# Kernel tuning notes

Hardware: AMD Instinct MI355X
Metric: run time of the kernel (lower is better)

The kernel has to match this reference:

```python
import jax, jax.numpy as jnp
import numpy as np
from math import sqrt

EPS = 1e-5
N_BISECT = 30

def _entmax15_impl(x):
    # alpha=1.5 entmax along last axis via bisection (entmax_bisect, alpha=1.5)
    xs = x * 0.5  # (alpha-1) * x
    mx = jnp.max(xs, axis=-1, keepdims=True)
    d = xs.shape[-1]
    lo = mx - 1.0
    hi = mx - d ** -0.5  # d^{-(alpha-1)}
    def body(i, carry):
        lo, hi = carry
        mid = 0.5 * (lo + hi)
        f = jnp.sum(jnp.square(jnp.maximum(xs - mid, 0.0)), -1, keepdims=True) - 1.0
        lo = jnp.where(f > 0, mid, lo)
        hi = jnp.where(f > 0, hi, mid)
        return lo, hi
    lo, hi = jax.lax.fori_loop(0, N_BISECT, body, (lo, hi))
    tau = 0.5 * (lo + hi)
    p = jnp.square(jnp.maximum(xs - tau, 0.0))
    return p / jnp.sum(p, -1, keepdims=True)

@jax.custom_vjp
def entmax15(x):
    return _entmax15_impl(x)

def _entmax15_fwd(x):
    p = _entmax15_impl(x)
    return p, p

def _entmax15_bwd(p, g):
    # exact entmax-1.5 backward (entmax repo): gppr = sqrt(p) on support
    s = jnp.sqrt(p)
    dx = g * s
    q = jnp.sum(dx, -1, keepdims=True) / jnp.sum(s, -1, keepdims=True)
    return (dx - q * s,)

entmax15.defvjp(_entmax15_fwd, _entmax15_bwd)

def layer_norm(x, g, b):
    m = jnp.mean(x, -1, keepdims=True)
    v = jnp.var(x, -1, keepdims=True)
    return (x - m) / jnp.sqrt(v + EPS) * g + b

def mlp(x, w1, b1, w2, b2):
    return jax.nn.gelu(x @ w1 + b1, approximate=False) @ w2 + b2

def hopfield_core(q_in, k_in, H, wq, bq, wk, bk, wv, bv, wo, bo):
    # Faithful to Hopfield.forward with mix=True; `values` arg of the torch
    # module is ignored (it recomputes value_projection(key_projection(keys))).
    B, L, _ = q_in.shape
    S = k_in.shape[1]
    q = (q_in @ wq + bq).reshape(B, L, H, -1)
    k = k_in @ wk + bk
    v = (k @ wv + bv).reshape(B, S, H, -1)
    kh = k.reshape(B, S, H, -1)
    E = q.shape[-1]
    scores = jnp.einsum('blhe,bshe->bhls', q, kh) * (1.0 / sqrt(E))
    A = entmax15(scores)
    out = jnp.einsum('bhls,bshd->blhd', A, v)
    # mix=True: transpose(2,1) then view(B, L, -1) on contiguous (B,H,L,D)
    out = jnp.transpose(out, (0, 2, 1, 3)).reshape(B, L, -1)
    return out @ wo + bo

def _forward(n_heads, x, ct_wq, ct_bq, ct_wk, ct_bk, ct_wv, ct_bv, ct_wo, ct_bo,
             cs_wq, cs_bq, cs_wk, cs_bk, cs_wv, cs_bv, cs_wo, cs_bo, cs_key,
             hp_wq, hp_bq, hp_wk, hp_bk, hp_wv, hp_bv, hp_wo, hp_bo,
             n1_g, n1_b, n2_g, n2_b, n3_g, n3_b, n4_g, n4_b,
             m1_w1, m1_b1, m1_w2, m1_b2, m2_w1, m2_b1, m2_w2, m2_b2):
    b, ts_d, seg, d = x.shape
    time_in = x.reshape(b * ts_d, seg, d)
    time_enc = hopfield_core(time_in, time_in, n_heads,
                             ct_wq, ct_bq, ct_wk, ct_bk, ct_wv, ct_bv, ct_wo, ct_bo)
    dim_in = layer_norm(time_in + time_enc, n1_g, n1_b)
    dim_in = layer_norm(dim_in + mlp(dim_in, m1_w1, m1_b1, m1_w2, m1_b2), n2_g, n2_b)
    # '(b ts_d) seg d -> (b seg) ts_d d'
    series_in = dim_in.reshape(b, ts_d, seg, d).transpose(0, 2, 1, 3).reshape(b * seg, ts_d, d)
    # HopfieldPooling: learned stored patterns as keys
    pooled_keys = jnp.broadcast_to(cs_key, (b * seg,) + cs_key.shape[1:])
    series_h = hopfield_core(series_in, pooled_keys, n_heads,
                             cs_wq, cs_bq, cs_wk, cs_bk, cs_wv, cs_bv, cs_wo, cs_bo)
    pooled_h = hopfield_core(series_in, series_in, n_heads,
                             hp_wq, hp_bq, hp_wk, hp_bk, hp_wv, hp_bv, hp_wo, hp_bo)
    dim_enc = layer_norm(series_h + pooled_h, n3_g, n3_b)
    dim_enc = layer_norm(dim_enc + mlp(dim_enc, m2_w1, m2_b1, m2_w2, m2_b2), n4_g, n4_b)
    # '(b seg) ts_d d -> b ts_d seg d'
    return dim_enc.reshape(b, seg, ts_d, d).transpose(0, 2, 1, 3)

def setup_inputs() -> dict:
    b, ts_d, seg, d, h, dff, factor = 8, 32, 64, 1024, 16, 4096, 10
    keys = iter(jax.random.split(jax.random.key(0), 64))
    def rn(shape, s=0.02):
        return jax.random.normal(next(keys), shape, jnp.float32) * s
    inp = {"x": jax.random.normal(next(keys), (b, ts_d, seg, d), jnp.float32)}
    for p in ("ct", "cs", "hp"):
        inp[p + "_wq"] = rn((d, d)); inp[p + "_bq"] = rn((d,))
        inp[p + "_wk"] = rn((d, d)); inp[p + "_bk"] = rn((d,))
        inp[p + "_wv"] = rn((d, d)); inp[p + "_bv"] = rn((d,))
        inp[p + "_wo"] = rn((d, d)); inp[p + "_bo"] = rn((d,))
    inp["cs_key"] = rn((1, factor, d), 0.1)
    for i in ("1", "2", "3", "4"):
        inp["n" + i + "_g"] = jnp.ones((d,), jnp.float32)
        inp["n" + i + "_b"] = jnp.zeros((d,), jnp.float32)
    for m in ("m1", "m2"):
        inp[m + "_w1"] = rn((d, dff)); inp[m + "_b1"] = rn((dff,))
        inp[m + "_w2"] = rn((dff, d)); inp[m + "_b2"] = rn((d,))
    inp["n_heads"] = h
    return inp

def reference(x, ct_wq, ct_bq, ct_wk, ct_bk, ct_wv, ct_bv, ct_wo, ct_bo,
              cs_wq, cs_bq, cs_wk, cs_bk, cs_wv, cs_bv, cs_wo, cs_bo, cs_key,
              hp_wq, hp_bq, hp_wk, hp_bk, hp_wv, hp_bv, hp_wo, hp_bo,
              n1_g, n1_b, n2_g, n2_b, n3_g, n3_b, n4_g, n4_b,
              m1_w1, m1_b1, m1_w2, m1_b2, m2_w1, m2_b1, m2_w2, m2_b2, n_heads):
    return _forward(n_heads, x, ct_wq, ct_bq, ct_wk, ct_bk, ct_wv, ct_bv, ct_wo, ct_bo,
                    cs_wq, cs_bq, cs_wk, cs_bk, cs_wv, cs_bv, cs_wo, cs_bo, cs_key,
                    hp_wq, hp_bq, hp_wk, hp_bk, hp_wv, hp_bv, hp_wo, hp_bo,
                    n1_g, n1_b, n2_g, n2_b, n3_g, n3_b, n4_g, n4_b,
                    m1_w1, m1_b1, m1_w2, m1_b2, m2_w1, m2_b1, m2_w2, m2_b2)
```

## Files before the change

### kernel.cpp

```cpp
#include <hip/hip_runtime.h>
#include <cstdio>

typedef __bf16 bf16x8 __attribute__((ext_vector_type(8)));
typedef float f32x4 __attribute__((ext_vector_type(4)));
typedef int i32x4 __attribute__((ext_vector_type(4)));
typedef unsigned short u16x4 __attribute__((ext_vector_type(4)));

__device__ __forceinline__ float bf2f(unsigned short u) {
  union { unsigned int i; float f; } x; x.i = ((unsigned int)u) << 16; return x.f;
}
__device__ __forceinline__ unsigned short f2bf(float f) {
  union { float f; unsigned int i; } x; x.f = f;
  unsigned int r = x.i + 0x7fffu + ((x.i >> 16) & 1u);
  return (unsigned short)(r >> 16);
}

__device__ __forceinline__ void gl2lds16(const unsigned short* g, unsigned short* l) {
  __builtin_amdgcn_global_load_lds((const __attribute__((address_space(1))) unsigned int*)g,
                                   (__attribute__((address_space(3))) unsigned int*)l, 16, 0, 0);
}

__global__ __launch_bounds__(256) void k_cast(const float* __restrict__ in,
                                              unsigned short* __restrict__ out, int n4) {
  int i = blockIdx.x * 256 + threadIdx.x;
  if (i >= n4) return;
  f32x4 v = ((const f32x4*)in)[i];
  u16x4 o;
  o[0] = f2bf(v[0]); o[1] = f2bf(v[1]); o[2] = f2bf(v[2]); o[3] = f2bf(v[3]);
  ((u16x4*)out)[i] = o;
}

__global__ __launch_bounds__(256) void k_tcast(const float* __restrict__ src,
                                               unsigned short* __restrict__ dst,
                                               int K, int N) {
  __shared__ float tile[32][33];
  int gx = blockIdx.x * 32;
  int gy = blockIdx.y * 32;
  int t = threadIdx.x;
  int c = t & 31, r0 = t >> 5;
#pragma unroll
  for (int i = 0; i < 4; i++) {
    int r = r0 + i * 8;
    tile[r][c] = src[(size_t)(gy + r) * N + gx + c];
  }
  __syncthreads();
#pragma unroll
  for (int i = 0; i < 4; i++) {
    int r = r0 + i * 8;
    dst[(size_t)(gx + r) * K + gy + c] = f2bf(tile[c][r]);
  }
}

template <bool GELU>
__global__ __launch_bounds__(256) void k_gemm(const unsigned short* __restrict__ A,
                                              const unsigned short* __restrict__ Bt,
                                              const float* __restrict__ bias,
                                              unsigned short* __restrict__ C,
                                              int M, int N, int K) {
  __shared__ unsigned short As[2][128 * 32];
  __shared__ unsigned short Bs[2][128 * 32];
  const int rowA0 = blockIdx.y * 128, colB0 = blockIdx.x * 128;
  const int t = threadIdx.x, w = t >> 6, lane = t & 63;
  const int wr = w >> 1, wc = w & 1;
  const int srow = w * 16 + (lane >> 2);
  const unsigned short* pa = A + (size_t)(rowA0 + srow) * K + (lane & 3) * 8;
  const unsigned short* pb = Bt + (size_t)(colB0 + srow) * K + (lane & 3) * 8;
  const size_t row64 = (size_t)64 * K;

  f32x4 acc[4][4] = {};
  const int ka = (lane >> 4) * 8, ra = lane & 15;

  auto stage = [&](int buf, int kk) {
    gl2lds16(pa + kk,         &As[buf][w * 512]);
    gl2lds16(pa + row64 + kk, &As[buf][2048 + w * 512]);
    gl2lds16(pb + kk,         &Bs[buf][w * 512]);
    gl2lds16(pb + row64 + kk, &Bs[buf][2048 + w * 512]);
  };
  stage(0, 0);
  int buf = 0;
  for (int kk = 0; kk < K; kk += 32) {
    asm volatile("s_waitcnt vmcnt(0)" ::: "memory");
    __syncthreads();
    if (kk + 32 < K) stage(buf ^ 1, kk + 32);
    bf16x8 af[4], bfr[4];
#pragma unroll
    for (int m = 0; m < 4; m++)
      af[m] = *(const bf16x8*)&As[buf][(wr * 64 + m * 16 + ra) * 32 + ka];
#pragma unroll
    for (int n = 0; n < 4; n++)
      bfr[n] = *(const bf16x8*)&Bs[buf][(wc * 64 + n * 16 + ra) * 32 + ka];
#pragma unroll
    for (int m = 0; m < 4; m++)
#pragma unroll
      for (int n = 0; n < 4; n++)
        acc[m][n] = __builtin_amdgcn_mfma_f32_16x16x32_bf16(af[m], bfr[n], acc[m][n], 0, 0, 0);
    buf ^= 1;
  }

  const int cr = (lane >> 4) * 4;
  const int cc = lane & 15;
#pragma unroll
  for (int m = 0; m < 4; m++) {
    int grow = rowA0 + wr * 64 + m * 16 + cr;
#pragma unroll
    for (int n = 0; n < 4; n++) {
      int gcol = colB0 + wc * 64 + n * 16 + cc;
      float bv = bias[gcol];
#pragma unroll
      for (int i = 0; i < 4; i++) {
        float v = acc[m][n][i] + bv;
        if (GELU) v = 0.5f * v * (1.f + erff(v * 0.70710678118654752f));
        C[(size_t)(grow + i) * N + gcol] = f2bf(v);
      }
    }
  }
}

__global__ __launch_bounds__(256) void k_gemm10(const unsigned short* __restrict__ A,
                                                const unsigned short* __restrict__ Bt,
                                                const float* __restrict__ bias,
                                                unsigned short* __restrict__ C) {
  __shared__ float af[1024];
  int m = blockIdx.x, nb = blockIdx.y;
  int t = threadIdx.x;
#pragma unroll
  for (int i = 0; i < 4; i++) af[t * 4 + i] = bf2f(A[(size_t)m * 1024 + t * 4 + i]);
  __syncthreads();
  int w = t >> 6, lane = t & 63;
  for (int n = nb * 64 + w; n < nb * 64 + 64; n += 4) {
    const unsigned short* brow = Bt + (size_t)n * 1024 + lane * 16;
    float acc = 0.f;
#pragma unroll
    for (int j = 0; j < 16; j++) acc += af[lane * 16 + j] * bf2f(brow[j]);
#pragma unroll
    for (int o = 32; o; o >>= 1) acc += __shfl_xor(acc, o);
    if (lane == 0) C[(size_t)m * 1024 + n] = f2bf(acc + bias[n]);
  }
}

template <int L, int S, bool SHARED>
__global__ __launch_bounds__(256) void k_attn(const unsigned short* __restrict__ Q,
                                              const unsigned short* __restrict__ Kb,
                                              const unsigned short* __restrict__ Vb,
                                              unsigned short* __restrict__ Out) {
  constexpr int SP = (S <= 32) ? 32 : 64;
  constexpr int QST = 72;
  constexpr int VST = SP + 8;
  constexpr int CST = SP + 4;
  __shared__ unsigned short Qs[L * QST];
  __shared__ unsigned short Ks[SP * QST];
  __shared__ unsigned short Vt[64 * VST];
  __shared__ float Sc[L * CST];
  __shared__ float Rps[L];
  const int blk = blockIdx.x, batch = blk >> 4, h = blk & 15;
  const int t = threadIdx.x, w = t >> 6, lane = t & 63;

  for (int c = t; c < L * 8; c += 256) {
    int r = c >> 3, ch = (c & 7) * 8;
    *(i32x4*)&Qs[r * QST + ch] =
        *(const i32x4*)&Q[((size_t)(batch * L + r)) * 1024 + h * 64 + ch];
  }
  for (int c = t; c < SP * 8; c += 256) {
    int r = c >> 3, ch = (c & 7) * 8;
    i32x4 v = {0, 0, 0, 0};
    if (r < S) {
      size_t rb = SHARED ? (size_t)r : (size_t)(batch * S + r);
      v = *(const i32x4*)&Kb[rb * 1024 + h * 64 + ch];
    }
    *(i32x4*)&Ks[r * QST + ch] = v;
  }
  for (int c = t; c < SP * 64; c += 256) {
    int s = c >> 6, e = c & 63;
    unsigned short v = 0;
    if (s < S) {
      size_t rb = SHARED ? (size_t)s : (size_t)(batch * S + s);
      v = Vb[rb * 1024 + h * 64 + e];
    }
    Vt[e * VST + s] = v;
  }
  __syncthreads();

  const int ka = (lane >> 4) * 8, ra = lane & 15;
  const int cr = (lane >> 4) * 4, cc = lane & 15;
  constexpr int NT = SP / 16, TT = (L / 16) * NT;
  for (int tt = w; tt < TT; tt += 4) {
    int m = tt / NT, n = tt % NT;
    f32x4 a = {0.f, 0.f, 0.f, 0.f};
#pragma unroll
    for (int ks = 0; ks < 2; ks++) {
      bf16x8 af = *(const bf16x8*)&Qs[(m * 16 + ra) * QST + ks * 32 + ka];
      bf16x8 bf = *(const bf16x8*)&Ks[(n * 16 + ra) * QST + ks * 32 + ka];
      a = __builtin_amdgcn_mfma_f32_16x16x32_bf16(af, bf, a, 0, 0, 0);
    }
#pragma unroll
    for (int i = 0; i < 4; i++)
      Sc[(m * 16 + cr + i) * CST + n * 16 + cc] = a[i] * 0.0625f;
  }
  __syncthreads();

  constexpr int G = 256 / L, RW = 64 / G, SL = SP / G;
  const int row = w * RW + lane / G, sub = lane % G;
  float xs[SL];
#pragma unroll
  for (int j = 0; j < SL; j++) {
    int s = sub * SL + j;
    float v = Sc[row * CST + s];
    if (S < SP && s >= S) v = -1e30f;
    xs[j] = v;
  }
  float mx = xs[0];
#pragma unroll
  for (int j = 1; j < SL; j++) mx = fmaxf(mx, xs[j]);
#pragma unroll
  for (int o = G / 2; o; o >>= 1) mx = fmaxf(mx, __shfl_xor(mx, o));
  const float hoff = (S == 64) ? 0.125f : (S == 32) ? 0.17677669529663687f : 0.31622776601683794f;
  float lo = mx - 1.f, hi = mx - hoff;
#pragma unroll 1
  for (int it = 0; it < 26; it++) {
    float mid = 0.5f * (lo + hi);
    float f = 0.f;
#pragma unroll
    for (int j = 0; j < SL; j++) { float dd = fmaxf(xs[j] - mid, 0.f); f += dd * dd; }
#pragma unroll
    for (int o = G / 2; o; o >>= 1) f += __shfl_xor(f, o);
    bool gt = f > 1.f;
    lo = gt ? mid : lo;
    hi = gt ? hi : mid;
  }
  float tau = 0.5f * (lo + hi);
  float ps = 0.f;
#pragma unroll
  for (int j = 0; j < SL; j++) { float dd = fmaxf(xs[j] - tau, 0.f); xs[j] = dd * dd; ps += xs[j]; }
#pragma unroll
  for (int o = G / 2; o; o >>= 1) ps += __shfl_xor(ps, o);
  if (sub == 0) Rps[row] = 1.f / ps;
  unsigned short* Pb = Qs;
#pragma unroll
  for (int j = 0; j < SL; j += 4) {
    u16x4 pv;
#pragma unroll
    for (int jj = 0; jj < 4; jj++) pv[jj] = f2bf(xs[j + jj]);
    *(u16x4*)&Pb[row * VST + sub * SL + j] = pv;
  }
  __syncthreads();

  constexpr int TT2 = (L / 16) * 4;
  for (int tt = w; tt < TT2; tt += 4) {
    int m = tt >> 2, n = tt & 3;
    f32x4 a = {0.f, 0.f, 0.f, 0.f};
#pragma unroll
    for (int ks = 0; ks < SP / 32; ks++) {
      bf16x8 af = *(const bf16x8*)&Pb[(m * 16 + ra) * VST + ks * 32 + ka];
      bf16x8 bf = *(const bf16x8*)&Vt[(n * 16 + ra) * VST + ks * 32 + ka];
      a = __builtin_amdgcn_mfma_f32_16x16x32_bf16(af, bf, a, 0, 0, 0);
    }
#pragma unroll
    for (int i = 0; i < 4; i++) {
      int l = m * 16 + cr + i, e = n * 16 + cc;
      float val = a[i] * Rps[l];
      int l_new = h * (L / 16) + (l >> 4);
      int cg = (l & 15) * 64 + e;
      Out[((size_t)(batch * L + l_new)) * 1024 + cg] = f2bf(val);
    }
  }
}

template <int MODE, bool F32OUT>
__global__ __launch_bounds__(256) void k_ln(const unsigned short* __restrict__ a,
                                            const unsigned short* __restrict__ b,
                                            const float* __restrict__ g,
                                            const float* __restrict__ be,
                                            void* __restrict__ outp) {
  __shared__ float red[8];
  int r = blockIdx.x, t = threadIdx.x;
  size_t base = (size_t)r * 1024 + t * 4;
  u16x4 av = *(const u16x4*)(a + base);
  u16x4 bv = *(const u16x4*)(b + base);
  float x[4];
  float s = 0.f, ss = 0.f;
#pragma unroll
  for (int i = 0; i < 4; i++) {
    x[i] = bf2f(av[i]) + bf2f(bv[i]);
    s += x[i]; ss += x[i] * x[i];
  }
#pragma unroll
  for (int o = 32; o; o >>= 1) { s += __shfl_xor(s, o); ss += __shfl_xor(ss, o); }
  int w = t >> 6;
  if ((t & 63) == 0) { red[w] = s; red[4 + w] = ss; }
  __syncthreads();
  s = red[0] + red[1] + red[2] + red[3];
  ss = red[4] + red[5] + red[6] + red[7];
  float mean = s * (1.f / 1024.f);
  float var = ss * (1.f / 1024.f) - mean * mean;
  float rstd = rsqrtf(var + 1e-5f);
  int orow;
  if (MODE == 0) orow = r;
  else if (MODE == 1) { int bi = r >> 11, rem = r & 2047; int tt = rem >> 6, sd = rem & 63; orow = (bi << 11) + sd * 32 + tt; }
  else { int bi = r >> 11, rem = r & 2047; int sd = rem >> 5, tt = rem & 31; orow = (bi << 11) + tt * 64 + sd; }
  size_t ob = (size_t)orow * 1024 + t * 4;
  if (F32OUT) {
    f32x4 y;
#pragma unroll
    for (int i = 0; i < 4; i++) y[i] = (x[i] - mean) * rstd * g[t * 4 + i] + be[t * 4 + i];
    *(f32x4*)((float*)outp + ob) = y;
  } else {
    u16x4 y;
#pragma unroll
    for (int i = 0; i < 4; i++) y[i] = f2bf((x[i] - mean) * rstd * g[t * 4 + i] + be[t * 4 + i]);
    *(u16x4*)((unsigned short*)outp + ob) = y;
  }
}


extern "C" void kernel_launch(void* const* d_in, const int* in_sizes, int n_in,
                              void* d_out, int out_size, void* d_ws, size_t ws_size,
                              hipStream_t stream) {
  const int M = 16384;
  if (n_in < 43 || in_sizes[0] != 16777216 || in_sizes[25] != 10240 || in_sizes[34] != 4194304) {
    fprintf(stderr, "kernel_launch: unexpected input layout (n_in=%d s0=%d s25=%d s34=%d)\n",
            n_in, in_sizes[0], n_in > 25 ? in_sizes[25] : -1, n_in > 34 ? in_sizes[34] : -1);
    return;
  }
  const float* x = (const float*)d_in[0];
  const float* w[3][4]; const float* bia[3][4];
  for (int p = 0; p < 3; p++) {
    w[p][0] = (const float*)d_in[1 + 8 * p + 0]; bia[p][0] = (const float*)d_in[1 + 8 * p + 1];
    w[p][1] = (const float*)d_in[1 + 8 * p + 2]; bia[p][1] = (const float*)d_in[1 + 8 * p + 3];
    w[p][2] = (const float*)d_in[1 + 8 * p + 4]; bia[p][2] = (const float*)d_in[1 + 8 * p + 5];
    w[p][3] = (const float*)d_in[1 + 8 * p + 6]; bia[p][3] = (const float*)d_in[1 + 8 * p + 7];
  }
  const float* cs_key = (const float*)d_in[25];
  const float* ng[4]; const float* nb[4];
  for (int i = 0; i < 4; i++) { ng[i] = (const float*)d_in[26 + 2 * i]; nb[i] = (const float*)d_in[27 + 2 * i]; }
  const float* m_w1[2]; const float* m_b1[2]; const float* m_w2[2]; const float* m_b2[2];
  for (int i = 0; i < 2; i++) {
    m_w1[i] = (const float*)d_in[34 + 4 * i]; m_b1[i] = (const float*)d_in[35 + 4 * i];
    m_w2[i] = (const float*)d_in[36 + 4 * i]; m_b2[i] = (const float*)d_in[37 + 4 * i];
  }

  char* base = (char*)d_ws; size_t off = 0;
  auto alloc = [&](size_t bytes) -> void* {
    off = (off + 255) & ~(size_t)255;
    void* p = base + off; off += bytes; return p;
  };
  unsigned short* Wt[3][4];
  for (int p = 0; p < 3; p++)
    for (int j = 0; j < 4; j++) Wt[p][j] = (unsigned short*)alloc((size_t)1024 * 1024 * 2);
  unsigned short* Wm1u = (unsigned short*)alloc((size_t)4096 * 1024 * 2);
  unsigned short* Wm1d = (unsigned short*)alloc((size_t)1024 * 4096 * 2);
  unsigned short* Wm2u = (unsigned short*)alloc((size_t)4096 * 1024 * 2);
  unsigned short* Wm2d = (unsigned short*)alloc((size_t)1024 * 4096 * 2);
  unsigned short* A[5];
  for (int i = 0; i < 5; i++) A[i] = (unsigned short*)alloc((size_t)M * 1024 * 2);
  unsigned short* KeyB = (unsigned short*)alloc((size_t)10 * 1024 * 2);
  unsigned short* Kcs = (unsigned short*)alloc((size_t)10 * 1024 * 2);
  unsigned short* Vcs = (unsigned short*)alloc((size_t)10 * 1024 * 2);
  if (off > ws_size) {
    fprintf(stderr, "kernel_launch: ws too small: need %zu have %zu\n", off, ws_size);
    return;
  }
  const int MC = 8192;
  unsigned short* HbT = A[0];
  unsigned short* HbS = A[1];

  auto gemm = [&](const unsigned short* Ap, const unsigned short* Bt, const float* bi,
                  unsigned short* Cp, int Mm, int Nn, int Kk, bool gelu) {
    dim3 g(Nn / 128, Mm / 128);
    if (gelu) k_gemm<true><<<g, 256, 0, stream>>>(Ap, Bt, bi, Cp, Mm, Nn, Kk);
    else      k_gemm<false><<<g, 256, 0, stream>>>(Ap, Bt, bi, Cp, Mm, Nn, Kk);
  };

  for (int p = 0; p < 3; p++)
    for (int j = 0; j < 4; j++)
      k_tcast<<<dim3(32, 32), 256, 0, stream>>>(w[p][j], Wt[p][j], 1024, 1024);
  k_tcast<<<dim3(128, 32), 256, 0, stream>>>(m_w1[0], Wm1u, 1024, 4096);
  k_tcast<<<dim3(32, 128), 256, 0, stream>>>(m_w2[0], Wm1d, 4096, 1024);
  k_tcast<<<dim3(128, 32), 256, 0, stream>>>(m_w1[1], Wm2u, 1024, 4096);
  k_tcast<<<dim3(32, 128), 256, 0, stream>>>(m_w2[1], Wm2d, 4096, 1024);
  k_cast<<<16384, 256, 0, stream>>>(x, A[0], 16777216 / 4);
  k_cast<<<10, 256, 0, stream>>>(cs_key, KeyB, 10240 / 4);

  gemm(A[0], Wt[0][1], bia[0][1], A[1], M, 1024, 1024, false);
  gemm(A[0], Wt[0][0], bia[0][0], A[2], M, 1024, 1024, false);
  gemm(A[1], Wt[0][2], bia[0][2], A[3], M, 1024, 1024, false);
  k_attn<64, 64, false><<<256 * 16, 256, 0, stream>>>(A[2], A[1], A[3], A[4]);
  gemm(A[4], Wt[0][3], bia[0][3], A[1], M, 1024, 1024, false);
  k_ln<0, false><<<M, 256, 0, stream>>>(A[0], A[1], ng[0], nb[0], A[2]);
  for (int c = 0; c < M; c += MC) {
    gemm(A[2] + (size_t)c * 1024, Wm1u, m_b1[0], HbT, MC, 4096, 1024, true);
    gemm(HbT, Wm1d, m_b2[0], A[4] + (size_t)c * 1024, MC, 1024, 4096, false);
  }
  k_ln<1, false><<<M, 256, 0, stream>>>(A[2], A[4], ng[1], nb[1], A[3]);

  k_gemm10<<<dim3(10, 16), 256, 0, stream>>>(KeyB, Wt[1][1], bia[1][1], Kcs);
  k_gemm10<<<dim3(10, 16), 256, 0, stream>>>(Kcs, Wt[1][2], bia[1][2], Vcs);
  gemm(A[3], Wt[1][0], bia[1][0], A[0], M, 1024, 1024, false);
  k_attn<32, 10, true><<<512 * 16, 256, 0, stream>>>(A[0], Kcs, Vcs, A[1]);
  gemm(A[1], Wt[1][3], bia[1][3], A[2], M, 1024, 1024, false);
  gemm(A[3], Wt[2][1], bia[2][1], A[0], M, 1024, 1024, false);
  gemm(A[3], Wt[2][0], bia[2][0], A[1], M, 1024, 1024, false);
  gemm(A[0], Wt[2][2], bia[2][2], A[4], M, 1024, 1024, false);
  k_attn<32, 32, false><<<512 * 16, 256, 0, stream>>>(A[1], A[0], A[4], A[3]);
  gemm(A[3], Wt[2][3], bia[2][3], A[1], M, 1024, 1024, false);
  k_ln<0, false><<<M, 256, 0, stream>>>(A[2], A[1], ng[2], nb[2], A[0]);
  for (int c = 0; c < M; c += MC) {
    gemm(A[0] + (size_t)c * 1024, Wm2u, m_b1[1], HbS, MC, 4096, 1024, true);
    gemm(HbS, Wm2d, m_b2[1], A[3] + (size_t)c * 1024, MC, 1024, 4096, false);
  }
  k_ln<2, true><<<M, 256, 0, stream>>>(A[0], A[3], ng[3], nb[3], d_out);
}
```

Baseline: 1.772 ms.

## Triple-buffer GEMM LDS loads, XOR-swizzle LDS layout, and vectorize epilogue stores

The bf16 MFMA GEMM now uses three LDS stages and prefetches two tiles ahead, waiting with partial vmcnt instead of draining all loads each iteration. The LDS tile layout is XOR-swizzled on both the global-to-LDS write and the fragment reads to reduce bank conflicts. The epilogue stages each 16x64 output slice through LDS so every lane writes 16-byte vectorized rows instead of scattered 2-byte stores. This uses more shared memory, which may reduce occupancy, and adds an extra barrier per k-step.

```diff
diff --git a/kernel.cpp b/kernel.cpp
--- a/kernel.cpp
+++ b/kernel.cpp
@@ -57,18 +57,20 @@
                                               const float* __restrict__ bias,
                                               unsigned short* __restrict__ C,
                                               int M, int N, int K) {
-  __shared__ unsigned short As[2][128 * 32];
-  __shared__ unsigned short Bs[2][128 * 32];
+  __shared__ unsigned short As[3][128 * 32];
+  __shared__ unsigned short Bs[3][128 * 32];
   const int rowA0 = blockIdx.y * 128, colB0 = blockIdx.x * 128;
   const int t = threadIdx.x, w = t >> 6, lane = t & 63;
   const int wr = w >> 1, wc = w & 1;
   const int srow = w * 16 + (lane >> 2);
-  const unsigned short* pa = A + (size_t)(rowA0 + srow) * K + (lane & 3) * 8;
-  const unsigned short* pb = Bt + (size_t)(colB0 + srow) * K + (lane & 3) * 8;
+  const int schunk = (lane & 3) ^ ((lane >> 3) & 3);
+  const unsigned short* pa = A + (size_t)(rowA0 + srow) * K + schunk * 8;
+  const unsigned short* pb = Bt + (size_t)(colB0 + srow) * K + schunk * 8;
   const size_t row64 = (size_t)64 * K;
 
   f32x4 acc[4][4] = {};
-  const int ka = (lane >> 4) * 8, ra = lane & 15;
+  const int g = lane >> 4, ra = lane & 15;
+  const int gp8 = (g ^ ((ra >> 1) & 3)) * 8;
 
   auto stage = [&](int buf, int kk) {
     gl2lds16(pa + kk,         &As[buf][w * 512]);
@@ -76,43 +78,65 @@
     gl2lds16(pb + kk,         &Bs[buf][w * 512]);
     gl2lds16(pb + row64 + kk, &Bs[buf][2048 + w * 512]);
   };
+
+  const int NT = K >> 5;
   stage(0, 0);
-  int buf = 0;
-  for (int kk = 0; kk < K; kk += 32) {
-    asm volatile("s_waitcnt vmcnt(0)" ::: "memory");
+  if (NT > 1) stage(1, 32);
+  int cur = 0;
+  for (int j = 0; j < NT; ++j) {
+    if (j + 2 < NT) {
+      int nxt2 = cur + 2; if (nxt2 >= 3) nxt2 -= 3;
+      stage(nxt2, (j + 2) * 32);
+      asm volatile("s_waitcnt vmcnt(8)" ::: "memory");
+    } else if (j + 1 < NT) {
+      asm volatile("s_waitcnt vmcnt(4)" ::: "memory");
+    } else {
+      asm volatile("s_waitcnt vmcnt(0)" ::: "memory");
+    }
     __syncthreads();
-    if (kk + 32 < K) stage(buf ^ 1, kk + 32);
     bf16x8 af[4], bfr[4];
 #pragma unroll
     for (int m = 0; m < 4; m++)
-      af[m] = *(const bf16x8*)&As[buf][(wr * 64 + m * 16 + ra) * 32 + ka];
+      af[m] = *(const bf16x8*)&As[cur][(wr * 64 + m * 16 + ra) * 32 + gp8];
 #pragma unroll
     for (int n = 0; n < 4; n++)
-      bfr[n] = *(const bf16x8*)&Bs[buf][(wc * 64 + n * 16 + ra) * 32 + ka];
+      bfr[n] = *(const bf16x8*)&Bs[cur][(wc * 64 + n * 16 + ra) * 32 + gp8];
 #pragma unroll
     for (int m = 0; m < 4; m++)
 #pragma unroll
       for (int n = 0; n < 4; n++)
         acc[m][n] = __builtin_amdgcn_mfma_f32_16x16x32_bf16(af[m], bfr[n], acc[m][n], 0, 0, 0);
-    buf ^= 1;
-  }
-
-  const int cr = (lane >> 4) * 4;
-  const int cc = lane & 15;
+    __syncthreads();
+    cur += 1; if (cur >= 3) cur -= 3;
+  }
+
+  unsigned short* Ep = &As[0][0] + w * 1024;
+  const int grow0 = rowA0 + wr * 64;
+  const int gcol0 = colB0 + wc * 64;
+  float bv[4];
+#pragma unroll
+  for (int n = 0; n < 4; n++) bv[n] = bias[gcol0 + n * 16 + ra];
+  const int rdrow = lane >> 3, rg = lane & 7;
 #pragma unroll
   for (int m = 0; m < 4; m++) {
-    int grow = rowA0 + wr * 64 + m * 16 + cr;
-#pragma unroll
-    for (int n = 0; n < 4; n++) {
-      int gcol = colB0 + wc * 64 + n * 16 + cc;
-      float bv = bias[gcol];
+#pragma unroll
+    for (int n = 0; n < 4; n++)
 #pragma unroll
       for (int i = 0; i < 4; i++) {
-        float v = acc[m][n][i] + bv;
+        int r = g * 4 + i;
+        float v = acc[m][n][i] + bv[n];
         if (GELU) v = 0.5f * v * (1.f + erff(v * 0.70710678118654752f));
-        C[(size_t)(grow + i) * N + gcol] = f2bf(v);
+        Ep[r * 64 + ((ra + n * 16) ^ ((r & 7) << 3))] = f2bf(v);
       }
-    }
+    asm volatile("s_waitcnt lgkmcnt(0)" ::: "memory");
+    __builtin_amdgcn_sched_barrier(0);
+#pragma unroll
+    for (int p = 0; p < 2; p++) {
+      int rr = p * 8 + rdrow;
+      bf16x8 val = *(const bf16x8*)&Ep[rr * 64 + ((rg ^ (rr & 7)) << 3)];
+      *(bf16x8*)&C[(size_t)(grow0 + m * 16 + rr) * N + gcol0 + rg * 8] = val;
+    }
+    asm volatile("s_waitcnt lgkmcnt(0)" ::: "memory");
   }
 }
 
@@ -365,9 +389,9 @@
 
   auto gemm = [&](const unsigned short* Ap, const unsigned short* Bt, const float* bi,
                   unsigned short* Cp, int Mm, int Nn, int Kk, bool gelu) {
-    dim3 g(Nn / 128, Mm / 128);
-    if (gelu) k_gemm<true><<<g, 256, 0, stream>>>(Ap, Bt, bi, Cp, Mm, Nn, Kk);
-    else      k_gemm<false><<<g, 256, 0, stream>>>(Ap, Bt, bi, Cp, Mm, Nn, Kk);
+    dim3 gg(Nn / 128, Mm / 128);
+    if (gelu) k_gemm<true><<<gg, 256, 0, stream>>>(Ap, Bt, bi, Cp, Mm, Nn, Kk);
+    else      k_gemm<false><<<gg, 256, 0, stream>>>(Ap, Bt, bi, Cp, Mm, Nn, Kk);
   };
 
   for (int p = 0; p < 3; p++)
```

After: 1.759 ms. About the same (-0.8%).
